# Optimization experiments

Hardware: AMD Instinct MI355X
Metric: run time of the kernel (lower is better)

Reference implementation:

```python
import jax, jax.numpy as jnp
import numpy as np

NEG_INF = -1e9
LEAKY_SLOPE = 0.2


def setup_inputs() -> dict:
    key = jax.random.key(0)
    k1, k2, k3, k4, k5 = jax.random.split(key, 5)
    B, N, F_in, F_out = 8, 2048, 256, 256
    x = jax.random.normal(k1, (B, N, F_in), dtype=jnp.float32)
    adj = jax.random.randint(k2, (B, N, N), 0, 2, dtype=jnp.int32)
    W = jax.random.normal(k3, (F_out, F_in), dtype=jnp.float32) * 0.05
    a_src = jax.random.normal(k4, (F_out,), dtype=jnp.float32) * 0.05
    a_dst = jax.random.normal(k5, (F_out,), dtype=jnp.float32) * 0.05
    return {"x": x, "adj": adj, "W": W, "a_src": a_src, "a_dst": a_dst}


def reference(x, adj, W, a_src, a_dst):
    # h: (B, N, F_out)
    h = jnp.einsum("bnf,of->bno", x, W)
    # a([h_i ; h_j]) == h_i @ a_src + h_j @ a_dst  (avoids O(N^2, 2F) concat)
    s_src = h @ a_src  # (B, N) score contribution of row node i
    s_dst = h @ a_dst  # (B, N) score contribution of col node j
    e = s_src[:, :, None] + s_dst[:, None, :]  # (B, N, N)
    e = jax.nn.leaky_relu(e, negative_slope=LEAKY_SLOPE)
    e = jnp.where(adj == 0, jnp.float32(NEG_INF), e)
    alpha = jax.nn.softmax(e, axis=-1)  # dropout is identity in eval mode
    h_prime = jnp.einsum("bij,bjo->bio", alpha, h)
    return h_prime
```

## Files before the change

### kernel.cpp

```cpp
#include <hip/hip_runtime.h>
#include <hip/hip_bf16.h>
#include <cstdint>
#include <cstddef>

typedef __attribute__((ext_vector_type(8))) short short8;
typedef __attribute__((ext_vector_type(4))) short short4v;
typedef __attribute__((ext_vector_type(4))) float floatx4;
typedef __attribute__((ext_vector_type(16))) float floatx16;
typedef unsigned short ushort_t;
typedef unsigned long long u64_t;

#define LOG2E 1.44269504088896340736f

__device__ __forceinline__ unsigned short f2bf(float f) {
    unsigned u = __float_as_uint(f);
    u += 0x7FFFu + ((u >> 16) & 1u);
    return (unsigned short)(u >> 16);
}
__device__ __forceinline__ float bf2f(unsigned short s) {
    return __uint_as_float(((unsigned)s) << 16);
}

__global__ __launch_bounds__(1024) void gemm_h(const float* __restrict__ x,
                                               const float* __restrict__ W,
                                               const int* __restrict__ adj,
                                               ushort_t* __restrict__ hT,
                                               const float* __restrict__ a_src,
                                               const float* __restrict__ a_dst,
                                               float* __restrict__ s_src,
                                               float* __restrict__ s_dst,
                                               u64_t* __restrict__ adjb) {
    const int tid = threadIdx.x;
    const int w = tid >> 6, lane = tid & 63;
    const int q = lane >> 4, t16 = lane & 15;
    const int jg = w >> 2, og = w & 3;

    __shared__ ushort_t wt[256][72];
    __shared__ float sred[2][4][64];

    const int jrow = blockIdx.x * 64 + jg * 16 + t16;
    const float* xr = x + (size_t)jrow * 256 + q * 8;
    short8 af[8];
#pragma unroll
    for (int kb = 0; kb < 8; ++kb) {
        float4 v0 = *(const float4*)(xr + kb * 32);
        float4 v1 = *(const float4*)(xr + kb * 32 + 4);
        short8 a;
        a[0] = (short)f2bf(v0.x); a[1] = (short)f2bf(v0.y);
        a[2] = (short)f2bf(v0.z); a[3] = (short)f2bf(v0.w);
        a[4] = (short)f2bf(v1.x); a[5] = (short)f2bf(v1.y);
        a[6] = (short)f2bf(v1.z); a[7] = (short)f2bf(v1.w);
        af[kb] = a;
    }

    floatx4 acc[4] = {};
#pragma unroll
    for (int kp = 0; kp < 4; ++kp) {
        if (kp) __syncthreads();
#pragma unroll
        for (int r = 0; r < 2; ++r) {
            int G = tid + 1024 * r;
            int row = G >> 3, g = G & 7;
            const float* wsrc = W + (size_t)row * 256 + kp * 64 + g * 8;
            float4 f0 = *(const float4*)(wsrc);
            float4 f1 = *(const float4*)(wsrc + 4);
            short8 wv;
            wv[0] = (short)f2bf(f0.x); wv[1] = (short)f2bf(f0.y);
            wv[2] = (short)f2bf(f0.z); wv[3] = (short)f2bf(f0.w);
            wv[4] = (short)f2bf(f1.x); wv[5] = (short)f2bf(f1.y);
            wv[6] = (short)f2bf(f1.z); wv[7] = (short)f2bf(f1.w);
            *(short8*)(&wt[row][g * 8]) = wv;
        }
        __syncthreads();
#pragma unroll
        for (int ks = 0; ks < 2; ++ks) {
#pragma unroll
            for (int ct = 0; ct < 4; ++ct) {
                short8 bf = *(const short8*)(&wt[og * 64 + ct * 16 + t16][ks * 32 + q * 8]);
                acc[ct] = __builtin_amdgcn_mfma_f32_16x16x32_bf16(af[kp * 2 + ks], bf, acc[ct], 0, 0, 0);
            }
        }
    }

    const int jbase = blockIdx.x * 64 + jg * 16 + q * 4;
    const int b = jbase >> 11, jj = jbase & 2047;
#pragma unroll
    for (int ct = 0; ct < 4; ++ct) {
        const int o = og * 64 + ct * 16 + t16;
        short4v sv;
        sv[0] = (short)f2bf(acc[ct][0]);
        sv[1] = (short)f2bf(acc[ct][1]);
        sv[2] = (short)f2bf(acc[ct][2]);
        sv[3] = (short)f2bf(acc[ct][3]);
        *(short4v*)(hT + ((size_t)b * 256 + o) * 2048 + jj) = sv;
    }

    float psv[4] = {}, pdv[4] = {};
#pragma unroll
    for (int ct = 0; ct < 4; ++ct) {
        const int o = og * 64 + ct * 16 + t16;
        float as = a_src[o], ad = a_dst[o];
#pragma unroll
        for (int r = 0; r < 4; ++r) {
            psv[r] = __fmaf_rn(acc[ct][r], as, psv[r]);
            pdv[r] = __fmaf_rn(acc[ct][r], ad, pdv[r]);
        }
    }
#pragma unroll
    for (int m = 1; m < 16; m <<= 1) {
#pragma unroll
        for (int r = 0; r < 4; ++r) {
            psv[r] += __shfl_xor(psv[r], m);
            pdv[r] += __shfl_xor(pdv[r], m);
        }
    }
    if (t16 == 0) {
#pragma unroll
        for (int r = 0; r < 4; ++r) {
            sred[0][og][jg * 16 + q * 4 + r] = psv[r];
            sred[1][og][jg * 16 + q * 4 + r] = pdv[r];
        }
    }
    __syncthreads();
    if (tid < 64) {
        float ss = sred[0][0][tid] + sred[0][1][tid] + sred[0][2][tid] + sred[0][3][tid];
        float dd = sred[1][0][tid] + sred[1][1][tid] + sred[1][2][tid] + sred[1][3][tid];
        s_src[blockIdx.x * 64 + tid] = ss;
        s_dst[blockIdx.x * 64 + tid] = dd;
    }

    {
        const int row0 = blockIdx.x * 64 + w * 4;
#pragma unroll
        for (int rr = 0; rr < 4; ++rr) {
            const int* ap = adj + (size_t)(row0 + rr) * 2048 + lane;
            u64_t* bp = adjb + (size_t)(row0 + rr) * 32;
#pragma unroll 4
            for (int g = 0; g < 32; ++g) {
                u64_t mk = __ballot(ap[g * 64] != 0);
                if (lane == 0) bp[g] = mk;
            }
        }
    }
}

__global__ __launch_bounds__(1024) void attn(const ushort_t* __restrict__ hT,
                                             const u64_t* __restrict__ adjb,
                                             const float* __restrict__ s_src,
                                             const float* __restrict__ s_dst,
                                             float* __restrict__ out) {
    const int tid = threadIdx.x;
    const int w = tid >> 6;
    const int lane = tid & 63;
    const int l5 = lane & 31, hi = lane >> 5;
    const int b = blockIdx.x;
    const int i0 = blockIdx.y * 64;

    __shared__ ushort_t hts[2][256][40];
    __shared__ ushort_t ps[2][64][40];
    __shared__ float sdl[2048];
    __shared__ float rls[64];

    const float* sdb = s_dst + (size_t)b * 2048;
    {
        int idx = tid * 2;
        float2 v = *(const float2*)(sdb + idx);
        v.x *= LOG2E; v.y *= LOG2E;
        *(float2*)(&sdl[idx]) = v;
    }

    const int ip = w * 4 + (lane >> 4);
    const int jp = lane & 15;
    const float si = s_src[(size_t)b * 2048 + i0 + ip] * LOG2E;
    const uint2* amr = (const uint2*)(adjb + ((size_t)b * 2048 + i0 + ip) * 32);

    const int hrow = tid >> 2, hseg = tid & 3;
    const ushort_t* hTg = hT + ((size_t)b * 256 + hrow) * 2048 + hseg * 8;

    const int osub = (w & 7) * 32, ih = (w >> 3) * 32;

    floatx16 acc = {};
    float lsum = 0.f;
    int4 hreg;
    uint2 amc, amcN;

    hreg = *(const int4*)(hTg);
    amc = amr[0];
    __syncthreads();

#pragma unroll 1
    for (int it = 0; it < 32; ++it) {
        const int c = it * 2;
        *(int4*)(&hts[0][hrow][hseg * 8]) = hreg;
        hreg = *(const int4*)(hTg + (size_t)(c + 1) * 32);
        amcN = amr[(it + 1 < 32) ? it + 1 : 31];
        {
            float2 sd = *(const float2*)(&sdl[c * 32 + jp * 2]);
            unsigned m0 = (amc.x >> (jp * 2)) & 1u;
            unsigned m1 = (amc.x >> (jp * 2 + 1)) & 1u;
            float t0 = si + sd.x;
            float t1 = si + sd.y;
            float l0 = fmaxf(t0, 0.2f * t0);
            float l1 = fmaxf(t1, 0.2f * t1);
            float p0 = __builtin_amdgcn_exp2f(l0);
            float p1 = __builtin_amdgcn_exp2f(l1);
            p0 = m0 ? p0 : 0.0f;
            p1 = m1 ? p1 : 0.0f;
            unsigned short u0 = f2bf(p0);
            unsigned short u1 = f2bf(p1);
            lsum += bf2f(u0) + bf2f(u1);
            *(unsigned*)(&ps[0][ip][jp * 2]) = (unsigned)u0 | ((unsigned)u1 << 16);
        }
        __syncthreads();
#pragma unroll
        for (int ks = 0; ks < 2; ++ks) {
            short8 afr = *(const short8*)(&hts[0][osub + l5][ks * 16 + hi * 8]);
            short8 bfr = *(const short8*)(&ps[0][ih + l5][ks * 16 + hi * 8]);
            acc = __builtin_amdgcn_mfma_f32_32x32x16_bf16(afr, bfr, acc, 0, 0, 0);
        }
        *(int4*)(&hts[1][hrow][hseg * 8]) = hreg;
        {
            const int nh = (c + 2 < 64) ? c + 2 : 63;
            hreg = *(const int4*)(hTg + (size_t)nh * 32);
        }
        {
            float2 sd = *(const float2*)(&sdl[(c + 1) * 32 + jp * 2]);
            unsigned m0 = (amc.y >> (jp * 2)) & 1u;
            unsigned m1 = (amc.y >> (jp * 2 + 1)) & 1u;
            float t0 = si + sd.x;
            float t1 = si + sd.y;
            float l0 = fmaxf(t0, 0.2f * t0);
            float l1 = fmaxf(t1, 0.2f * t1);
            float p0 = __builtin_amdgcn_exp2f(l0);
            float p1 = __builtin_amdgcn_exp2f(l1);
            p0 = m0 ? p0 : 0.0f;
            p1 = m1 ? p1 : 0.0f;
            unsigned short u0 = f2bf(p0);
            unsigned short u1 = f2bf(p1);
            lsum += bf2f(u0) + bf2f(u1);
            *(unsigned*)(&ps[1][ip][jp * 2]) = (unsigned)u0 | ((unsigned)u1 << 16);
        }
        __syncthreads();
#pragma unroll
        for (int ks = 0; ks < 2; ++ks) {
            short8 afr = *(const short8*)(&hts[1][osub + l5][ks * 16 + hi * 8]);
            short8 bfr = *(const short8*)(&ps[1][ih + l5][ks * 16 + hi * 8]);
            acc = __builtin_amdgcn_mfma_f32_32x32x16_bf16(afr, bfr, acc, 0, 0, 0);
        }
        amc = amcN;
    }

#pragma unroll
    for (int m = 1; m < 16; m <<= 1) lsum += __shfl_xor(lsum, m);
    if (jp == 0) rls[ip] = lsum;
    __syncthreads();

    {
        const int i = ih + l5;
        const float s = rls[i];
        const float rl = (s > 0.f) ? 1.0f / s : 0.0f;
        float* orow = out + ((size_t)b * 2048 + i0 + i) * 256 + osub;
#pragma unroll
        for (int rq = 0; rq < 4; ++rq) {
            floatx4 v;
            v[0] = acc[rq * 4 + 0] * rl;
            v[1] = acc[rq * 4 + 1] * rl;
            v[2] = acc[rq * 4 + 2] * rl;
            v[3] = acc[rq * 4 + 3] * rl;
            *(floatx4*)(orow + rq * 8 + hi * 4) = v;
        }
    }
}

extern "C" void kernel_launch(void* const* d_in, const int* in_sizes, int n_in,
                              void* d_out, int out_size, void* d_ws, size_t ws_size,
                              hipStream_t stream) {
    const float* x     = (const float*)d_in[0];
    const int*   adj   = (const int*)d_in[1];
    const float* W     = (const float*)d_in[2];
    const float* a_src = (const float*)d_in[3];
    const float* a_dst = (const float*)d_in[4];
    float* out = (float*)d_out;

    char* ws = (char*)d_ws;
    ushort_t* hT = (ushort_t*)ws;
    float* s_src = (float*)(ws + (size_t)8 * 1024 * 1024);
    float* s_dst = s_src + 16384;
    u64_t* adjb  = (u64_t*)(s_dst + 16384);

    gemm_h<<<256, 1024, 0, stream>>>(x, W, adj, hT, a_src, a_dst, s_src, s_dst, adjb);
    attn<<<dim3(8, 32), 1024, 0, stream>>>(hT, adjb, s_src, s_dst, out);
}
```

Before: 298.8 us.

## Split adjacency bit-packing into its own wide kernel and stage x tiles in LDS

```diff
diff --git a/kernel.cpp b/kernel.cpp
--- a/kernel.cpp
+++ b/kernel.cpp
@@ -21,37 +21,33 @@
     return __uint_as_float(((unsigned)s) << 16);
 }
 
+__global__ __launch_bounds__(256) void adjpack(const int* __restrict__ adj,
+                                               u64_t* __restrict__ adjb) {
+    const int w = threadIdx.x >> 6, lane = threadIdx.x & 63;
+    const size_t wbase = ((size_t)blockIdx.x * 4 + w) * 64;
+    const int* ap = adj + wbase * 64 + lane;
+#pragma unroll 8
+    for (int t = 0; t < 64; ++t) {
+        u64_t mk = __ballot(ap[(size_t)t * 64] != 0);
+        if (lane == 0) adjb[wbase + t] = mk;
+    }
+}
+
 __global__ __launch_bounds__(1024) void gemm_h(const float* __restrict__ x,
                                                const float* __restrict__ W,
-                                               const int* __restrict__ adj,
                                                ushort_t* __restrict__ hT,
                                                const float* __restrict__ a_src,
                                                const float* __restrict__ a_dst,
                                                float* __restrict__ s_src,
-                                               float* __restrict__ s_dst,
-                                               u64_t* __restrict__ adjb) {
+                                               float* __restrict__ s_dst) {
     const int tid = threadIdx.x;
     const int w = tid >> 6, lane = tid & 63;
-    const int q = lane >> 4, t16 = lane & 15;
+    const int q = (lane >> 4) & 3, t16 = lane & 15;
     const int jg = w >> 2, og = w & 3;
 
     __shared__ ushort_t wt[256][72];
+    __shared__ ushort_t xs[64][72];
     __shared__ float sred[2][4][64];
-
-    const int jrow = blockIdx.x * 64 + jg * 16 + t16;
-    const float* xr = x + (size_t)jrow * 256 + q * 8;
-    short8 af[8];
-#pragma unroll
-    for (int kb = 0; kb < 8; ++kb) {
-        float4 v0 = *(const float4*)(xr + kb * 32);
-        float4 v1 = *(const float4*)(xr + kb * 32 + 4);
-        short8 a;
-        a[0] = (short)f2bf(v0.x); a[1] = (short)f2bf(v0.y);
-        a[2] = (short)f2bf(v0.z); a[3] = (short)f2bf(v0.w);
-        a[4] = (short)f2bf(v1.x); a[5] = (short)f2bf(v1.y);
-        a[6] = (short)f2bf(v1.z); a[7] = (short)f2bf(v1.w);
-        af[kb] = a;
-    }
 
     floatx4 acc[4] = {};
 #pragma unroll
@@ -71,13 +67,22 @@
             wv[6] = (short)f2bf(f1.z); wv[7] = (short)f2bf(f1.w);
             *(short8*)(&wt[row][g * 8]) = wv;
         }
+        {
+            int row = tid >> 4, kc = (tid & 15) * 4;
+            float4 xv = *(const float4*)(x + (size_t)(blockIdx.x * 64 + row) * 256 + kp * 64 + kc);
+            short4v s;
+            s[0] = (short)f2bf(xv.x); s[1] = (short)f2bf(xv.y);
+            s[2] = (short)f2bf(xv.z); s[3] = (short)f2bf(xv.w);
+            *(short4v*)(&xs[row][kc]) = s;
+        }
         __syncthreads();
 #pragma unroll
         for (int ks = 0; ks < 2; ++ks) {
+            short8 af = *(const short8*)(&xs[jg * 16 + t16][ks * 32 + q * 8]);
 #pragma unroll
             for (int ct = 0; ct < 4; ++ct) {
                 short8 bf = *(const short8*)(&wt[og * 64 + ct * 16 + t16][ks * 32 + q * 8]);
-                acc[ct] = __builtin_amdgcn_mfma_f32_16x16x32_bf16(af[kp * 2 + ks], bf, acc[ct], 0, 0, 0);
+                acc[ct] = __builtin_amdgcn_mfma_f32_16x16x32_bf16(af, bf, acc[ct], 0, 0, 0);
             }
         }
     }
@@ -127,20 +132,6 @@
         float dd = sred[1][0][tid] + sred[1][1][tid] + sred[1][2][tid] + sred[1][3][tid];
         s_src[blockIdx.x * 64 + tid] = ss;
         s_dst[blockIdx.x * 64 + tid] = dd;
-    }
-
-    {
-        const int row0 = blockIdx.x * 64 + w * 4;
-#pragma unroll
-        for (int rr = 0; rr < 4; ++rr) {
-            const int* ap = adj + (size_t)(row0 + rr) * 2048 + lane;
-            u64_t* bp = adjb + (size_t)(row0 + rr) * 32;
-#pragma unroll 4
-            for (int g = 0; g < 32; ++g) {
-                u64_t mk = __ballot(ap[g * 64] != 0);
-                if (lane == 0) bp[g] = mk;
-            }
-        }
     }
 }
 
@@ -288,6 +279,7 @@
     float* s_dst = s_src + 16384;
     u64_t* adjb  = (u64_t*)(s_dst + 16384);
 
-    gemm_h<<<256, 1024, 0, stream>>>(x, W, adj, hT, a_src, a_dst, s_src, s_dst, adjb);
+    adjpack<<<2048, 256, 0, stream>>>(adj, adjb);
+    gemm_h<<<256, 1024, 0, stream>>>(x, W, hT, a_src, a_dst, s_src, s_dst);
     attn<<<dim3(8, 32), 1024, 0, stream>>>(hT, adjb, s_src, s_dst, out);
 }
```

Result: faster. 270.2 us (-9.6%).

## Split adjacency bit-packing into separate blocks with vectorized per-thread packing

Applied to the files above, without the earlier changes.

```diff
diff --git a/kernel.cpp b/kernel.cpp
--- a/kernel.cpp
+++ b/kernel.cpp
@@ -21,24 +21,47 @@
     return __uint_as_float(((unsigned)s) << 16);
 }
 
-__global__ __launch_bounds__(1024) void gemm_h(const float* __restrict__ x,
-                                               const float* __restrict__ W,
-                                               const int* __restrict__ adj,
-                                               ushort_t* __restrict__ hT,
-                                               const float* __restrict__ a_src,
-                                               const float* __restrict__ a_dst,
-                                               float* __restrict__ s_src,
-                                               float* __restrict__ s_dst,
-                                               u64_t* __restrict__ adjb) {
+__global__ __launch_bounds__(1024, 4) void prep(const float* __restrict__ x,
+                                                const float* __restrict__ W,
+                                                const int* __restrict__ adj,
+                                                ushort_t* __restrict__ hT,
+                                                const float* __restrict__ a_src,
+                                                const float* __restrict__ a_dst,
+                                                float* __restrict__ s_src,
+                                                float* __restrict__ s_dst,
+                                                u64_t* __restrict__ adjb) {
+    __shared__ ushort_t wt[256][72];
+    __shared__ float sred[2][4][64];
+
     const int tid = threadIdx.x;
     const int w = tid >> 6, lane = tid & 63;
+
+    if (blockIdx.x >= 256) {
+        const size_t w_idx = (size_t)(blockIdx.x - 256) * 1024 + tid;
+        const int* ap = adj + (w_idx << 6);
+        int4 a[16];
+#pragma unroll
+        for (int k = 0; k < 16; ++k)
+            a[k] = *(const int4*)(ap + k * 4);
+        u64_t out = 0;
+#pragma unroll
+        for (int m = 0; m < 8; ++m) {
+            const int4 lo = a[2 * m], hi = a[2 * m + 1];
+            unsigned v = (lo.x != 0 ? 1u : 0u)   | (lo.y != 0 ? 2u : 0u)  |
+                         (lo.z != 0 ? 4u : 0u)   | (lo.w != 0 ? 8u : 0u)  |
+                         (hi.x != 0 ? 16u : 0u)  | (hi.y != 0 ? 32u : 0u) |
+                         (hi.z != 0 ? 64u : 0u)  | (hi.w != 0 ? 128u : 0u);
+            out |= (u64_t)v << (8 * m);
+        }
+        adjb[w_idx] = out;
+        return;
+    }
+
+    const int bid = blockIdx.x;
     const int q = lane >> 4, t16 = lane & 15;
     const int jg = w >> 2, og = w & 3;
 
-    __shared__ ushort_t wt[256][72];
-    __shared__ float sred[2][4][64];
-
-    const int jrow = blockIdx.x * 64 + jg * 16 + t16;
+    const int jrow = bid * 64 + jg * 16 + t16;
     const float* xr = x + (size_t)jrow * 256 + q * 8;
     short8 af[8];
 #pragma unroll
@@ -82,7 +105,7 @@
         }
     }
 
-    const int jbase = blockIdx.x * 64 + jg * 16 + q * 4;
+    const int jbase = bid * 64 + jg * 16 + q * 4;
     const int b = jbase >> 11, jj = jbase & 2047;
 #pragma unroll
     for (int ct = 0; ct < 4; ++ct) {
@@ -125,22 +148,8 @@
     if (tid < 64) {
         float ss = sred[0][0][tid] + sred[0][1][tid] + sred[0][2][tid] + sred[0][3][tid];
         float dd = sred[1][0][tid] + sred[1][1][tid] + sred[1][2][tid] + sred[1][3][tid];
-        s_src[blockIdx.x * 64 + tid] = ss;
-        s_dst[blockIdx.x * 64 + tid] = dd;
-    }
-
-    {
-        const int row0 = blockIdx.x * 64 + w * 4;
-#pragma unroll
-        for (int rr = 0; rr < 4; ++rr) {
-            const int* ap = adj + (size_t)(row0 + rr) * 2048 + lane;
-            u64_t* bp = adjb + (size_t)(row0 + rr) * 32;
-#pragma unroll 4
-            for (int g = 0; g < 32; ++g) {
-                u64_t mk = __ballot(ap[g * 64] != 0);
-                if (lane == 0) bp[g] = mk;
-            }
-        }
+        s_src[bid * 64 + tid] = ss;
+        s_dst[bid * 64 + tid] = dd;
     }
 }
 
@@ -288,6 +297,6 @@
     float* s_dst = s_src + 16384;
     u64_t* adjb  = (u64_t*)(s_dst + 16384);
 
-    gemm_h<<<256, 1024, 0, stream>>>(x, W, adj, hT, a_src, a_dst, s_src, s_dst, adjb);
+    prep<<<768, 1024, 0, stream>>>(x, W, adj, hT, a_src, a_dst, s_src, s_dst, adjb);
     attn<<<dim3(8, 32), 1024, 0, stream>>>(hT, adjb, s_src, s_dst, out);
 }
```

Result: faster. 254.6 us (-14.8%).
